# Performance work log

Measured on AMD Instinct MI355X. Metric: run time of the kernel, lower is better.

The kernel has to match this reference:

```python
import jax, jax.numpy as jnp
import numpy as np

ALPHA = 0.5
NUM_CLASSES = 100
DIM = 512
BATCH = 65536


def setup_inputs() -> dict:
    key = jax.random.key(0)
    k1, k2, k3 = jax.random.split(key, 3)
    features = jax.random.normal(k1, (BATCH, DIM), dtype=jnp.float32)
    labels = jax.random.randint(k2, (BATCH,), 0, NUM_CLASSES)
    onehot = jax.nn.one_hot(labels, NUM_CLASSES, dtype=jnp.float32)  # [B, 100]
    # Keras 'uniform' initializer defaults to U(-0.05, 0.05)
    centers = jax.random.uniform(k3, (NUM_CLASSES, DIM), dtype=jnp.float32,
                                 minval=-0.05, maxval=0.05)
    return {"features": features, "onehot": onehot, "centers": centers}


def reference(features, onehot, centers):
    # selected_centers[b] = centers[label[b]] via one-hot matmul (as in original)
    selected = jnp.matmul(onehot, centers)                      # [B, DIM]
    diff = selected - features                                  # [B, DIM]
    # per-class scatter-add of diff, expressed as dense one-hot matmul
    delta_centers = jnp.matmul(onehot.T, diff)                  # [C, DIM]
    center_counts = jnp.sum(onehot, axis=0)[:, None] + 1.0      # [C, 1]
    delta_centers = delta_centers / center_counts
    new_centers = centers - ALPHA * delta_centers               # [C, DIM]
    # layer output: squared distance of each feature to its class center
    res = features - selected                                   # [B, DIM]
    result = jnp.sum(res * res, axis=1, keepdims=True)          # [B, 1]
    return result, new_centers
```

## Files before the change

kernel.cpp:

```cpp
#include <hip/hip_runtime.h>

#define BATCH 65536
#define DIM 512
#define NCLS 100
#define ALPHA 0.5f

#define CAP 1024
#define SORT_RPB 512
#define SORT_THREADS 256
#define CHUNKS 32
#define CBLOCK 256
#define SLOTS (CHUNKS * (CBLOCK / 64))

#define WS_COUNTS_OFF 0
#define WS_ORDER_OFF  512
#define WS_AUX_OFF    (512 + NCLS * CAP * 4)
#define WS_PART_BYTES (CHUNKS * NCLS * DIM * 4)

__global__ void __launch_bounds__(SORT_THREADS)
sort_kernel(const float* __restrict__ onehot,
            int* __restrict__ counts,
            int* __restrict__ order) {
    __shared__ int lhist[NCLS];
    __shared__ int lbase[NCLS];
    __shared__ short llab[SORT_RPB];
    __shared__ short lrank[SORT_RPB];

    const int t = threadIdx.x;
    const int r0 = blockIdx.x * SORT_RPB;

    for (int c = t; c < NCLS; c += SORT_THREADS) lhist[c] = 0;
    __syncthreads();

    const float4* oh4 = reinterpret_cast<const float4*>(onehot);
#pragma unroll
    for (int rr = 0; rr < SORT_RPB / SORT_THREADS; ++rr) {
        const int r = rr * SORT_THREADS + t;
        const int b = r0 + r;
        float lab = 0.0f;
#pragma unroll
        for (int j = 0; j < NCLS / 4; ++j) {
            const float4 v = oh4[b * (NCLS / 4) + j];
            lab += v.x * (float)(4 * j)
                 + v.y * (float)(4 * j + 1)
                 + v.z * (float)(4 * j + 2)
                 + v.w * (float)(4 * j + 3);
        }
        const int c = (int)(lab + 0.5f);
        llab[r] = (short)c;
        lrank[r] = (short)atomicAdd(&lhist[c], 1);
    }
    __syncthreads();

    for (int c = t; c < NCLS; c += SORT_THREADS)
        lbase[c] = atomicAdd(&counts[c], lhist[c]);
    __syncthreads();

#pragma unroll
    for (int rr = 0; rr < SORT_RPB / SORT_THREADS; ++rr) {
        const int r = rr * SORT_THREADS + t;
        const int c = llab[r];
        order[c * CAP + lbase[c] + lrank[r]] = r0 + r;
    }
}

__global__ void __launch_bounds__(CBLOCK)
delta_kernel(const float* __restrict__ features,
             const float* __restrict__ centers,
             const int* __restrict__ order,
             const int* __restrict__ counts,
             float* __restrict__ aux,
             float* __restrict__ result,
             const int use_part) {
    __shared__ float red[4][DIM];

    const int c = blockIdx.y;
    const int cnt = counts[c];
    const int lane = threadIdx.x & 63;
    const int wave = threadIdx.x >> 6;
    const int slot = blockIdx.x * (CBLOCK / 64) + wave;
    const int d = lane * 8;

    const float4 c0 = *reinterpret_cast<const float4*>(&centers[c * DIM + d]);
    const float4 c1 = *reinterpret_cast<const float4*>(&centers[c * DIM + d + 4]);
    float4 sA = make_float4(0.f, 0.f, 0.f, 0.f);
    float4 sB = make_float4(0.f, 0.f, 0.f, 0.f);

    const int* ord = &order[c * CAP];
    int i = slot;
    for (; i + SLOTS < cnt; i += 2 * SLOTS) {
        const int b0 = ord[i];
        const int b1 = ord[i + SLOTS];
        const float4 f00 = *reinterpret_cast<const float4*>(&features[b0 * DIM + d]);
        const float4 f01 = *reinterpret_cast<const float4*>(&features[b0 * DIM + d + 4]);
        const float4 f10 = *reinterpret_cast<const float4*>(&features[b1 * DIM + d]);
        const float4 f11 = *reinterpret_cast<const float4*>(&features[b1 * DIM + d + 4]);

        sA.x += f00.x + f10.x; sA.y += f00.y + f10.y;
        sA.z += f00.z + f10.z; sA.w += f00.w + f10.w;
        sB.x += f01.x + f11.x; sB.y += f01.y + f11.y;
        sB.z += f01.z + f11.z; sB.w += f01.w + f11.w;

        float dx, dy, dz, dw;
        dx = f00.x - c0.x; dy = f00.y - c0.y; dz = f00.z - c0.z; dw = f00.w - c0.w;
        float sq0 = dx * dx + dy * dy + dz * dz + dw * dw;
        dx = f01.x - c1.x; dy = f01.y - c1.y; dz = f01.z - c1.z; dw = f01.w - c1.w;
        sq0 += dx * dx + dy * dy + dz * dz + dw * dw;
        dx = f10.x - c0.x; dy = f10.y - c0.y; dz = f10.z - c0.z; dw = f10.w - c0.w;
        float sq1 = dx * dx + dy * dy + dz * dz + dw * dw;
        dx = f11.x - c1.x; dy = f11.y - c1.y; dz = f11.z - c1.z; dw = f11.w - c1.w;
        sq1 += dx * dx + dy * dy + dz * dz + dw * dw;

#pragma unroll
        for (int m = 32; m >= 1; m >>= 1) {
            sq0 += __shfl_xor(sq0, m);
            sq1 += __shfl_xor(sq1, m);
        }
        if (lane == 0) {
            result[b0] = sq0;
            result[b1] = sq1;
        }
    }
    if (i < cnt) {
        const int b = ord[i];
        const float4 f0 = *reinterpret_cast<const float4*>(&features[b * DIM + d]);
        const float4 f1 = *reinterpret_cast<const float4*>(&features[b * DIM + d + 4]);
        sA.x += f0.x; sA.y += f0.y; sA.z += f0.z; sA.w += f0.w;
        sB.x += f1.x; sB.y += f1.y; sB.z += f1.z; sB.w += f1.w;
        float dx, dy, dz, dw;
        dx = f0.x - c0.x; dy = f0.y - c0.y; dz = f0.z - c0.z; dw = f0.w - c0.w;
        float sq = dx * dx + dy * dy + dz * dz + dw * dw;
        dx = f1.x - c1.x; dy = f1.y - c1.y; dz = f1.z - c1.z; dw = f1.w - c1.w;
        sq += dx * dx + dy * dy + dz * dz + dw * dw;
#pragma unroll
        for (int m = 32; m >= 1; m >>= 1) sq += __shfl_xor(sq, m);
        if (lane == 0) result[b] = sq;
    }

    float* r = &red[wave][d];
    r[0] = sA.x; r[1] = sA.y; r[2] = sA.z; r[3] = sA.w;
    r[4] = sB.x; r[5] = sB.y; r[6] = sB.z; r[7] = sB.w;
    __syncthreads();

    const int t = threadIdx.x;
    if (use_part) {
        float* dst = &aux[(blockIdx.x * NCLS + c) * DIM];
#pragma unroll
        for (int k = 0; k < DIM / CBLOCK; ++k) {
            const int dd = k * CBLOCK + t;
            dst[dd] = red[0][dd] + red[1][dd] + red[2][dd] + red[3][dd];
        }
    } else {
#pragma unroll
        for (int k = 0; k < DIM / CBLOCK; ++k) {
            const int dd = k * CBLOCK + t;
            const float s = red[0][dd] + red[1][dd] + red[2][dd] + red[3][dd];
            unsafeAtomicAdd(&aux[c * DIM + dd], s);
        }
    }
}

__global__ void finalize_kernel(const float* __restrict__ centers,
                                const float* __restrict__ aux,
                                const int* __restrict__ counts,
                                float* __restrict__ new_centers,
                                const int use_part) {
    const int idx = blockIdx.x * blockDim.x + threadIdx.x;
    if (idx >= NCLS * DIM) return;
    float s;
    if (use_part) {
        s = 0.0f;
#pragma unroll
        for (int k = 0; k < CHUNKS; ++k) s += aux[k * NCLS * DIM + idx];
    } else {
        s = aux[idx];
    }
    const int c = idx >> 9;
    const float cntf = (float)counts[c];
    const float ctr = centers[idx];
    const float delta = (cntf * ctr - s) / (cntf + 1.0f);
    new_centers[idx] = ctr - ALPHA * delta;
}

extern "C" void kernel_launch(void* const* d_in, const int* in_sizes, int n_in,
                              void* d_out, int out_size, void* d_ws, size_t ws_size,
                              hipStream_t stream) {
    const float* features = (const float*)d_in[0];
    const float* onehot   = (const float*)d_in[1];
    const float* centers  = (const float*)d_in[2];

    float* result      = (float*)d_out;
    float* new_centers = (float*)d_out + BATCH;

    char* ws = (char*)d_ws;
    int*   counts = (int*)(ws + WS_COUNTS_OFF);
    int*   order  = (int*)(ws + WS_ORDER_OFF);
    float* aux    = (float*)(ws + WS_AUX_OFF);

    const int use_part = (ws_size >= (size_t)WS_AUX_OFF + WS_PART_BYTES) ? 1 : 0;

    hipMemsetAsync(counts, 0, 128 * sizeof(int), stream);
    if (!use_part)
        hipMemsetAsync(aux, 0, NCLS * DIM * sizeof(float), stream);

    sort_kernel<<<BATCH / SORT_RPB, SORT_THREADS, 0, stream>>>(onehot, counts, order);

    dim3 grid(CHUNKS, NCLS);
    delta_kernel<<<grid, CBLOCK, 0, stream>>>(features, centers, order, counts, aux, result, use_part);

    finalize_kernel<<<(NCLS * DIM + 255) / 256, 256, 0, stream>>>(centers, aux, counts, new_centers, use_part);
}
```

Measured before the change: 46.14 us.

## Batch all feature loads up front with fixed KMAX unroll and nontemporal loads

```diff
diff --git a/kernel.cpp b/kernel.cpp
--- a/kernel.cpp
+++ b/kernel.cpp
@@ -6,16 +6,19 @@
 #define ALPHA 0.5f
 
 #define CAP 1024
-#define SORT_RPB 512
+#define SORT_RPB 256
 #define SORT_THREADS 256
 #define CHUNKS 32
 #define CBLOCK 256
 #define SLOTS (CHUNKS * (CBLOCK / 64))
+#define KMAX 8
 
 #define WS_COUNTS_OFF 0
 #define WS_ORDER_OFF  512
 #define WS_AUX_OFF    (512 + NCLS * CAP * 4)
 #define WS_PART_BYTES (CHUNKS * NCLS * DIM * 4)
+
+typedef float f4v __attribute__((ext_vector_type(4)));
 
 __global__ void __launch_bounds__(SORT_THREADS)
 sort_kernel(const float* __restrict__ onehot,
@@ -33,10 +36,8 @@
     __syncthreads();
 
     const float4* oh4 = reinterpret_cast<const float4*>(onehot);
-#pragma unroll
-    for (int rr = 0; rr < SORT_RPB / SORT_THREADS; ++rr) {
-        const int r = rr * SORT_THREADS + t;
-        const int b = r0 + r;
+    {
+        const int b = r0 + t;
         float lab = 0.0f;
 #pragma unroll
         for (int j = 0; j < NCLS / 4; ++j) {
@@ -47,8 +48,8 @@
                  + v.w * (float)(4 * j + 3);
         }
         const int c = (int)(lab + 0.5f);
-        llab[r] = (short)c;
-        lrank[r] = (short)atomicAdd(&lhist[c], 1);
+        llab[t] = (short)c;
+        lrank[t] = (short)atomicAdd(&lhist[c], 1);
     }
     __syncthreads();
 
@@ -56,11 +57,9 @@
         lbase[c] = atomicAdd(&counts[c], lhist[c]);
     __syncthreads();
 
-#pragma unroll
-    for (int rr = 0; rr < SORT_RPB / SORT_THREADS; ++rr) {
-        const int r = rr * SORT_THREADS + t;
-        const int c = llab[r];
-        order[c * CAP + lbase[c] + lrank[r]] = r0 + r;
+    {
+        const int c = llab[t];
+        order[c * CAP + lbase[c] + lrank[t]] = r0 + t;
     }
 }
 
@@ -81,60 +80,41 @@
     const int slot = blockIdx.x * (CBLOCK / 64) + wave;
     const int d = lane * 8;
 
-    const float4 c0 = *reinterpret_cast<const float4*>(&centers[c * DIM + d]);
-    const float4 c1 = *reinterpret_cast<const float4*>(&centers[c * DIM + d + 4]);
-    float4 sA = make_float4(0.f, 0.f, 0.f, 0.f);
-    float4 sB = make_float4(0.f, 0.f, 0.f, 0.f);
+    const f4v c0 = *reinterpret_cast<const f4v*>(&centers[c * DIM + d]);
+    const f4v c1 = *reinterpret_cast<const f4v*>(&centers[c * DIM + d + 4]);
+    f4v sA = (f4v)(0.0f);
+    f4v sB = (f4v)(0.0f);
 
     const int* ord = &order[c * CAP];
-    int i = slot;
-    for (; i + SLOTS < cnt; i += 2 * SLOTS) {
-        const int b0 = ord[i];
-        const int b1 = ord[i + SLOTS];
-        const float4 f00 = *reinterpret_cast<const float4*>(&features[b0 * DIM + d]);
-        const float4 f01 = *reinterpret_cast<const float4*>(&features[b0 * DIM + d + 4]);
-        const float4 f10 = *reinterpret_cast<const float4*>(&features[b1 * DIM + d]);
-        const float4 f11 = *reinterpret_cast<const float4*>(&features[b1 * DIM + d + 4]);
+    int idx[KMAX];
+#pragma unroll
+    for (int k = 0; k < KMAX; ++k) idx[k] = ord[slot + k * SLOTS];
 
-        sA.x += f00.x + f10.x; sA.y += f00.y + f10.y;
-        sA.z += f00.z + f10.z; sA.w += f00.w + f10.w;
-        sB.x += f01.x + f11.x; sB.y += f01.y + f11.y;
-        sB.z += f01.z + f11.z; sB.w += f01.w + f11.w;
-
-        float dx, dy, dz, dw;
-        dx = f00.x - c0.x; dy = f00.y - c0.y; dz = f00.z - c0.z; dw = f00.w - c0.w;
-        float sq0 = dx * dx + dy * dy + dz * dz + dw * dw;
-        dx = f01.x - c1.x; dy = f01.y - c1.y; dz = f01.z - c1.z; dw = f01.w - c1.w;
-        sq0 += dx * dx + dy * dy + dz * dz + dw * dw;
-        dx = f10.x - c0.x; dy = f10.y - c0.y; dz = f10.z - c0.z; dw = f10.w - c0.w;
-        float sq1 = dx * dx + dy * dy + dz * dz + dw * dw;
-        dx = f11.x - c1.x; dy = f11.y - c1.y; dz = f11.z - c1.z; dw = f11.w - c1.w;
-        sq1 += dx * dx + dy * dy + dz * dz + dw * dw;
+    f4v F0[KMAX], F1[KMAX];
+#pragma unroll
+    for (int k = 0; k < KMAX; ++k) {
+        if (slot + k * SLOTS < cnt) {
+            const float* p = &features[(long)idx[k] * DIM + d];
+            F0[k] = __builtin_nontemporal_load(reinterpret_cast<const f4v*>(p));
+            F1[k] = __builtin_nontemporal_load(reinterpret_cast<const f4v*>(p + 4));
+        }
+    }
 
 #pragma unroll
-        for (int m = 32; m >= 1; m >>= 1) {
-            sq0 += __shfl_xor(sq0, m);
-            sq1 += __shfl_xor(sq1, m);
+    for (int k = 0; k < KMAX; ++k) {
+        if (slot + k * SLOTS < cnt) {
+            const f4v f0 = F0[k];
+            const f4v f1 = F1[k];
+            sA += f0;
+            sB += f1;
+            const f4v d0 = f0 - c0;
+            const f4v d1 = f1 - c1;
+            float sq = d0.x * d0.x + d0.y * d0.y + d0.z * d0.z + d0.w * d0.w
+                     + d1.x * d1.x + d1.y * d1.y + d1.z * d1.z + d1.w * d1.w;
+#pragma unroll
+            for (int m = 32; m >= 1; m >>= 1) sq += __shfl_xor(sq, m);
+            if (lane == 0) result[idx[k]] = sq;
         }
-        if (lane == 0) {
-            result[b0] = sq0;
-            result[b1] = sq1;
-        }
-    }
-    if (i < cnt) {
-        const int b = ord[i];
-        const float4 f0 = *reinterpret_cast<const float4*>(&features[b * DIM + d]);
-        const float4 f1 = *reinterpret_cast<const float4*>(&features[b * DIM + d + 4]);
-        sA.x += f0.x; sA.y += f0.y; sA.z += f0.z; sA.w += f0.w;
-        sB.x += f1.x; sB.y += f1.y; sB.z += f1.z; sB.w += f1.w;
-        float dx, dy, dz, dw;
-        dx = f0.x - c0.x; dy = f0.y - c0.y; dz = f0.z - c0.z; dw = f0.w - c0.w;
-        float sq = dx * dx + dy * dy + dz * dz + dw * dw;
-        dx = f1.x - c1.x; dy = f1.y - c1.y; dz = f1.z - c1.z; dw = f1.w - c1.w;
-        sq += dx * dx + dy * dy + dz * dz + dw * dw;
-#pragma unroll
-        for (int m = 32; m >= 1; m >>= 1) sq += __shfl_xor(sq, m);
-        if (lane == 0) result[b] = sq;
     }
 
     float* r = &red[wave][d];
```

After: 134.8 us. 192% more time.
